# Performance work log

Measured on AMD Instinct MI355X. Metric: run time of the kernel, lower is better.

The kernel has to match this reference:

```python
import jax, jax.numpy as jnp
import numpy as np

B, N, C, Q, H, RATIO = 8, 8700, 256, 300, 8, 4
D = C // H
HID = C * RATIO
EPS = 1e-5


def _ln(x, w, b):
    m = jnp.mean(x, axis=-1, keepdims=True)
    v = jnp.mean((x - m) ** 2, axis=-1, keepdims=True)
    return (x - m) * jax.lax.rsqrt(v + EPS) * w + b


def setup_inputs() -> dict:
    key = jax.random.key(0)
    ks = jax.random.split(key, 8)
    s = 0.02
    return {
        "x": jax.random.normal(ks[0], (B, N, C), jnp.float32),
        # linear weights stored [in, out] (y = x @ W), no biases (qkv_bias=False, Mlp bias=False)
        "Wq": jax.random.normal(ks[1], (C, C), jnp.float32) * s,
        "Wk": jax.random.normal(ks[2], (C, C), jnp.float32) * s,
        "Wv": jax.random.normal(ks[3], (C, C), jnp.float32) * s,
        "Wp": jax.random.normal(ks[4], (C, C), jnp.float32) * s,
        "W1": jax.random.normal(ks[5], (C, HID), jnp.float32) * s,
        "W2": jax.random.normal(ks[6], (HID, C), jnp.float32) * s,
        "ln1_w": jnp.ones((C,), jnp.float32),
        "ln1_b": jnp.zeros((C,), jnp.float32),
        "ln2_w": jnp.ones((C,), jnp.float32),
        "ln2_b": jnp.zeros((C,), jnp.float32),
        "gamma1": jnp.ones((C,), jnp.float32),
        "gamma2": jnp.ones((C,), jnp.float32),
    }


def reference(x, Wq, Wk, Wv, Wp, W1, W2, ln1_w, ln1_b, ln2_w, ln2_b, gamma1, gamma2):
    scale = D ** -0.5
    xn = _ln(x, ln1_w, ln1_b)                       # [B,N,C]
    # SAQAttn: queries only from the first Q tokens; keys/values from all N tokens
    q = (xn[:, :Q] @ Wq).reshape(B, Q, H, D) * scale  # [B,Q,H,D]
    k = (xn @ Wk).reshape(B, N, H, D)
    v = (xn @ Wv).reshape(B, N, H, D)
    attn = jax.nn.softmax(jnp.einsum('bqhd,bnhd->bhqn', q, k), axis=-1)  # [B,H,Q,N]
    x_det = jnp.einsum('bhqn,bnhd->bqhd', attn, v).reshape(B, Q, C) @ Wp  # [B,Q,C]
    # residual with layer-scale gamma1; context tokens pass normed features through
    x_attn = jnp.concatenate([x_det, xn[:, Q:]], axis=1)
    x = x + gamma1 * x_attn
    # tokens_norm=False: norm2 only on query tokens
    x = jnp.concatenate([_ln(x[:, :Q], ln2_w, ln2_b), x[:, Q:]], axis=1)
    # MLP on query tokens with layer-scale gamma2 (exact GELU, as nn.GELU default)
    det = gamma2 * (jax.nn.gelu(x[:, :Q] @ W1, approximate=False) @ W2)
    # faithful to source: x_res + cat([det, x[:,Q:]]) doubles the context tokens
    return x + jnp.concatenate([det, x[:, Q:]], axis=1)
```

## Files before the change

kernel.cpp:

```cpp
#include <hip/hip_runtime.h>

#define BB 8
#define NN 8700
#define CC 256
#define QQ 300
#define HH 8
#define DD 32
#define HIDN 1024
#define NSPLIT 16
#define TSTR (NSPLIT * 64)
#define KSLACK 1536
#define PADN (NN + KSLACK)

typedef unsigned short u16;
typedef __attribute__((ext_vector_type(8))) short short8;
typedef __attribute__((ext_vector_type(4))) float f32x4;

#define MFMA16(a, b, c) __builtin_amdgcn_mfma_f32_16x16x32_bf16((a), (b), (c), 0, 0, 0)

__device__ __forceinline__ unsigned int cvtpk(float lo, float hi) {
    unsigned int r;
    asm("v_cvt_pk_bf16_f32 %0, %1, %2" : "=v"(r) : "v"(lo), "v"(hi));
    return r;
}
__device__ __forceinline__ u16 f2b_hw(float f) { return (u16)cvtpk(f, 0.f); }
__device__ __forceinline__ float b2f(u16 u) {
    unsigned int x = ((unsigned int)u) << 16;
    return __builtin_bit_cast(float, x);
}
__device__ __forceinline__ void gload16(const u16* g, u16* l) {
    __builtin_amdgcn_global_load_lds(
        (const __attribute__((address_space(1))) void*)g,
        (__attribute__((address_space(3))) void*)l, 16, 0, 0);
}

__global__ __launch_bounds__(256)
void prep_k(const float* __restrict__ x, const float* __restrict__ ln1w,
            const float* __restrict__ ln1b, const float* __restrict__ g1,
            u16* __restrict__ xn, float* __restrict__ out,
            const float* __restrict__ Wq, const float* __restrict__ Wk,
            const float* __restrict__ Wv, const float* __restrict__ Wp,
            const float* __restrict__ W1, const float* __restrict__ W2,
            u16* __restrict__ wdst, float qscale)
{
    __shared__ u16 tl[64][66];
    if (blockIdx.x < 17400) {
        int row = blockIdx.x * 4 + (threadIdx.x >> 6);
        int l = threadIdx.x & 63;
        size_t base = (size_t)row * CC + l * 4;
        float4 xv = *reinterpret_cast<const float4*>(x + base);
        float s  = xv.x + xv.y + xv.z + xv.w;
        float s2 = xv.x * xv.x + xv.y * xv.y + xv.z * xv.z + xv.w * xv.w;
#pragma unroll
        for (int m = 1; m < 64; m <<= 1) {
            s  += __shfl_xor(s,  m, 64);
            s2 += __shfl_xor(s2, m, 64);
        }
        float mean = s * (1.0f / CC);
        float rs = rsqrtf(s2 * (1.0f / CC) - mean * mean + 1e-5f);
        float4 wv = *reinterpret_cast<const float4*>(ln1w + l * 4);
        float4 bb = *reinterpret_cast<const float4*>(ln1b + l * 4);
        float n0 = (xv.x - mean) * rs * wv.x + bb.x;
        float n1 = (xv.y - mean) * rs * wv.y + bb.y;
        float n2 = (xv.z - mean) * rs * wv.z + bb.z;
        float n3 = (xv.w - mean) * rs * wv.w + bb.w;
        uint2 u; u.x = cvtpk(n0, n1); u.y = cvtpk(n2, n3);
        *reinterpret_cast<uint2*>(xn + base) = u;
        int n = row % NN;
        if (n >= QQ) {
            float4 gv = *reinterpret_cast<const float4*>(g1 + l * 4);
            float4 o;
            o.x = 2.0f * (xv.x + gv.x * n0);
            o.y = 2.0f * (xv.y + gv.y * n1);
            o.z = 2.0f * (xv.z + gv.z * n2);
            o.w = 2.0f * (xv.w + gv.w * n3);
            *reinterpret_cast<float4*>(out + base) = o;
        }
    } else {
        int bid = blockIdx.x - 17400;
        const float* src; int K, N, tr, tc; size_t dof; float sc = 1.f;
        if (bid < 64) {
            int mat = bid >> 4, ti = bid & 15;
            src = (mat == 0) ? Wq : (mat == 1) ? Wk : (mat == 2) ? Wv : Wp;
            K = 256; N = 256; tr = ti >> 2; tc = ti & 3;
            dof = (size_t)mat * 65536;
            if (mat == 0) sc = qscale;
        } else if (bid < 128) {
            int ti = bid - 64; src = W1; K = 256; N = 1024; tr = ti >> 4; tc = ti & 15; dof = 262144;
        } else {
            int ti = bid - 128; src = W2; K = 1024; N = 256; tr = ti >> 2; tc = ti & 3; dof = 524288;
        }
        int tid = threadIdx.x;
        int jj = tid & 63;
        int i0 = tid >> 6;
#pragma unroll
        for (int ii = 0; ii < 16; ii++) {
            int kk = i0 * 16 + ii;
            float v = src[(size_t)(tr * 64 + kk) * N + tc * 64 + jj] * sc;
            tl[kk][jj] = f2b_hw(v);
        }
        __syncthreads();
#pragma unroll
        for (int ii = 0; ii < 16; ii++) {
            int nn = i0 * 16 + ii;
            wdst[dof + (size_t)(tc * 64 + nn) * K + tr * 64 + jj] = tl[jj][nn];
        }
    }
}

__global__ __launch_bounds__(512)
void gemm_kv(const u16* __restrict__ A, const u16* __restrict__ WT,
             u16* __restrict__ Cb, u16* __restrict__ Cb2, int M)
{
    __shared__ u16 alds[64 * 256];
    const int tid = threadIdx.x;
    const int w = tid >> 6, l = tid & 63;
    const int l15 = l & 15, kg = l >> 4;
    const int rowbase = blockIdx.x * 64;
    const f32x4 fz = {0.f, 0.f, 0.f, 0.f};

    {
        const char* gb = (const char*)(A + (size_t)rowbase * CC);
        char* lb = (char*)alds;
#pragma unroll
        for (int j = 0; j < 4; j++) {
            int o = tid * 64 + j * 16;
            short8 v = *reinterpret_cast<const short8*>(gb + o);
            int d = o ^ (((o >> 9) & 7) << 4);
            *reinterpret_cast<short8*>(lb + d) = v;
        }
    }
    __syncthreads();

    const int colbase = w * 64;
    const u16* bp[4];
#pragma unroll
    for (int ni = 0; ni < 4; ni++)
        bp[ni] = WT + (size_t)(colbase + ni * 16 + l15) * CC + kg * 8;

    f32x4 acc[4][4];
#pragma unroll
    for (int mi = 0; mi < 4; mi++)
#pragma unroll
        for (int ni = 0; ni < 4; ni++) acc[mi][ni] = fz;

    const char* lb = (const char*)alds;
    const int sw = (l15 & 7) << 4;
    int abase[4];
#pragma unroll
    for (int mi = 0; mi < 4; mi++) abase[mi] = (mi * 16 + l15) << 9;

#pragma unroll
    for (int ks = 0; ks < 8; ks++) {
        const int koff = ((ks * 64) + (kg * 16)) ^ sw;
        short8 a[4], bfr[4];
#pragma unroll
        for (int mi = 0; mi < 4; mi++)
            a[mi] = *reinterpret_cast<const short8*>(lb + abase[mi] + koff);
#pragma unroll
        for (int ni = 0; ni < 4; ni++)
            bfr[ni] = *reinterpret_cast<const short8*>(bp[ni] + ks * 32);
#pragma unroll
        for (int mi = 0; mi < 4; mi++)
#pragma unroll
            for (int ni = 0; ni < 4; ni++)
                acc[mi][ni] = MFMA16(bfr[ni], a[mi], acc[mi][ni]);
    }

#pragma unroll
    for (int mi = 0; mi < 4; mi++) {
        int r = rowbase + mi * 16 + l15;
        if (r >= M) continue;
        int bb = r / NN, n = r - bb * NN;
#pragma unroll
        for (int ni = 0; ni < 4; ni++) {
            int col0 = colbase + ni * 16 + kg * 4;
            f32x4 v = acc[mi][ni];
            uint2 pk; pk.x = cvtpk(v[0], v[1]); pk.y = cvtpk(v[2], v[3]);
            int c = (col0 < CC) ? col0 : col0 - CC;
            int hb = (c >> 5) * BB + bb;
            size_t off = ((size_t)hb * PADN + n) * DD + (c & 31);
            if (col0 < CC) *reinterpret_cast<uint2*>(Cb  + off) = pk;
            else           *reinterpret_cast<uint2*>(Cb2 + off) = pk;
        }
    }
}

__global__ __launch_bounds__(256)
void gemm_q(const u16* __restrict__ A, const u16* __restrict__ WT, u16* __restrict__ Cb, int M)
{
    const int w = threadIdx.x >> 6, l = threadIdx.x & 63;
    const int l15 = l & 15, kg = l >> 4;
    const int rowbase = blockIdx.x * 16;
    const int colbase = w * 64;
    const short8 z8 = {0, 0, 0, 0, 0, 0, 0, 0};
    const f32x4 fz = {0.f, 0.f, 0.f, 0.f};

    int r = rowbase + l15;
    bool av = (r < M);
    int rr = av ? r : 0;
    const u16* ap = A + ((size_t)(rr / QQ) * NN + (rr % QQ)) * CC + kg * 8;
    const u16* bp[4];
#pragma unroll
    for (int ni = 0; ni < 4; ni++)
        bp[ni] = WT + (size_t)(colbase + ni * 16 + l15) * CC + kg * 8;

    f32x4 acc[4];
#pragma unroll
    for (int ni = 0; ni < 4; ni++) acc[ni] = fz;

    for (int ks = 0; ks < CC; ks += 32) {
        short8 a = av ? *reinterpret_cast<const short8*>(ap + ks) : z8;
#pragma unroll
        for (int ni = 0; ni < 4; ni++) {
            short8 bfr = *reinterpret_cast<const short8*>(bp[ni] + ks);
            acc[ni] = MFMA16(bfr, a, acc[ni]);
        }
    }
    if (r < M) {
        int bb = r / QQ, q = r - bb * QQ;
#pragma unroll
        for (int ni = 0; ni < 4; ni++) {
            int col0 = colbase + ni * 16 + kg * 4;
            uint2 pk; pk.x = cvtpk(acc[ni][0], acc[ni][1]); pk.y = cvtpk(acc[ni][2], acc[ni][3]);
            int hb = (col0 >> 5) * BB + bb;
            *reinterpret_cast<uint2*>(Cb + ((size_t)hb * QQ + q) * DD + (col0 & 31)) = pk;
        }
    }
}

__global__ __launch_bounds__(256)
void attn_k(const u16* __restrict__ qm, const u16* __restrict__ km,
            const u16* __restrict__ vm, u16* __restrict__ Opb,
            float* __restrict__ lp)
{
    __shared__ u16 klds[2][64 * 32];
    __shared__ u16 vt[2][32 * 64];
    __shared__ u16 plds[4][2][16 * 64];

    const int bx = blockIdx.x;
    const int split = bx >> 6;
    const int rem = bx & 63;
    const int h = rem >> 3, b = rem & 7;
    const int bh = b * HH + h;
    const int hb = h * BB + b;
    const int tid = threadIdx.x;
    const int w = tid >> 6, l = tid & 63;
    const int l15 = l & 15, kg = l >> 4;
    const int tstart = split * 64;
    const int nt = (NN - tstart + TSTR - 1) / TSTR;

    const f32x4 fz = {0.f, 0.f, 0.f, 0.f};
    const short os = (short)0x3F80;
    const short8 ones = {os, os, os, os, os, os, os, os};

    const u16* kbase = km + (size_t)hb * PADN * DD;
    const u16* vbase = vm + (size_t)hb * PADN * DD;
    const u16* qbase = qm + (size_t)hb * QQ * DD;
    const int vkp = (tid & 31) * 2;
    const int vdg = (tid >> 5) * 4;

    const int krow  = (w << 4) + (l >> 2);
    const int kslot = (l & 3) ^ ((krow >> 1) & 3);
    const u16* ksrc = kbase + krow * DD + kslot * 8;

    short8 qfr[5];
#pragma unroll
    for (int qf = 0; qf < 5; qf++) {
        int qrow = w * 80 + qf * 16 + l15;
        int qc = qrow < QQ ? qrow : 0;
        qfr[qf] = *reinterpret_cast<const short8*>(qbase + (size_t)qc * DD + kg * 8);
    }

    f32x4 o[2][5]; float lpart[5];
#pragma unroll
    for (int qf = 0; qf < 5; qf++) { o[0][qf] = fz; o[1][qf] = fz; lpart[qf] = 0.f; }

    gload16(ksrc + (size_t)tstart * DD, (u16*)((char*)klds[0] + (w << 10)));
    ushort4 v0r = *reinterpret_cast<const ushort4*>(vbase + (size_t)(tstart + vkp) * DD + vdg);
    ushort4 v1r = *reinterpret_cast<const ushort4*>(vbase + (size_t)(tstart + vkp + 1) * DD + vdg);

    char* pl = (char*)plds[w];
    const int rdswz = ((l15 << 7) ^ ((l15 & 7) << 4)) + (kg << 4);
    const int wrbase = (l15 << 7) ^ ((l15 & 7) << 4);

    for (int t = 0; t < nt; ++t) {
        const int n0 = tstart + t * TSTR;
        char* vtb = (char*)vt[t & 1];
#pragma unroll
        for (int i = 0; i < 4; i++) {
            int row = vdg + i;
            unsigned int pk2 = (unsigned int)v0r[i] | ((unsigned int)v1r[i] << 16);
            int byteo = ((row << 7) + (vkp << 1)) ^ ((row & 7) << 4);
            *reinterpret_cast<unsigned int*>(vtb + byteo) = pk2;
        }
        __syncthreads();

        gload16(ksrc + (size_t)(n0 + TSTR) * DD, (u16*)((char*)klds[(t + 1) & 1] + (w << 10)));
        ushort4 v0n = *reinterpret_cast<const ushort4*>(vbase + (size_t)(n0 + TSTR + vkp) * DD + vdg);
        ushort4 v1n = *reinterpret_cast<const ushort4*>(vbase + (size_t)(n0 + TSTR + vkp + 1) * DD + vdg);

        short8 kf[4];
        { const char* klb = (const char*)klds[t & 1];
#pragma unroll
          for (int kb = 0; kb < 4; kb++) {
              int row = kb * 16 + l15;
              int off = (row << 6) + ((kg ^ ((row >> 1) & 3)) << 4);
              kf[kb] = *reinterpret_cast<const short8*>(klb + off);
          } }

        short8 va[2][2];
#pragma unroll
        for (int ks = 0; ks < 2; ks++)
#pragma unroll
            for (int dg = 0; dg < 2; dg++) {
                int row = dg * 16 + l15;
                int byteo = ((row << 7) + 64 * ks + 16 * kg) ^ ((row & 7) << 4);
                va[ks][dg] = *reinterpret_cast<const short8*>(vtb + byteo);
            }

        const bool tail = (n0 + 64 > NN);

#pragma unroll
        for (int qf = 0; qf < 5; qf++) {
            short8 bp0, bp1;
            if (qf > 0) {
                const char* plr = pl + (((qf - 1) & 1) << 11);
                bp0 = *reinterpret_cast<const short8*>(plr + rdswz);
                bp1 = *reinterpret_cast<const short8*>(plr + rdswz + 64);
            }
            f32x4 s[4];
            __builtin_amdgcn_s_setprio(1);
#pragma unroll
            for (int kb = 0; kb < 4; kb++)
                s[kb] = MFMA16(kf[kb], qfr[qf], fz);
            __builtin_amdgcn_s_setprio(0);
            char* plw = pl + ((qf & 1) << 11);
#pragma unroll
            for (int kb = 0; kb < 4; kb++) {
                float p0 = exp2f(s[kb][0]);
                float p1 = exp2f(s[kb][1]);
                float p2 = exp2f(s[kb][2]);
                float p3 = exp2f(s[kb][3]);
                if (tail) {
                    int kbase2 = n0 + 16 * kb + 4 * kg;
                    if (kbase2 + 0 >= NN) p0 = 0.f;
                    if (kbase2 + 1 >= NN) p1 = 0.f;
                    if (kbase2 + 2 >= NN) p2 = 0.f;
                    if (kbase2 + 3 >= NN) p3 = 0.f;
                }
                uint2 pw; pw.x = cvtpk(p0, p1); pw.y = cvtpk(p2, p3);
                *reinterpret_cast<uint2*>(plw + (wrbase + ((16 * kb + 4 * kg) << 1))) = pw;
            }
            if (qf > 0) {
                __builtin_amdgcn_s_setprio(1);
                o[0][qf - 1] = MFMA16(va[0][0], bp0, o[0][qf - 1]);
                o[1][qf - 1] = MFMA16(va[0][1], bp0, o[1][qf - 1]);
                o[0][qf - 1] = MFMA16(va[1][0], bp1, o[0][qf - 1]);
                o[1][qf - 1] = MFMA16(va[1][1], bp1, o[1][qf - 1]);
                f32x4 tsum = MFMA16(ones, bp0, fz);
                tsum = MFMA16(ones, bp1, tsum);
                __builtin_amdgcn_s_setprio(0);
                lpart[qf - 1] += tsum[0];
            }
        }
        {
            const char* plr = pl + 0;
            short8 bp0 = *reinterpret_cast<const short8*>(plr + rdswz);
            short8 bp1 = *reinterpret_cast<const short8*>(plr + rdswz + 64);
            __builtin_amdgcn_s_setprio(1);
            o[0][4] = MFMA16(va[0][0], bp0, o[0][4]);
            o[1][4] = MFMA16(va[0][1], bp0, o[1][4]);
            o[0][4] = MFMA16(va[1][0], bp1, o[0][4]);
            o[1][4] = MFMA16(va[1][1], bp1, o[1][4]);
            f32x4 tsum = MFMA16(ones, bp0, fz);
            tsum = MFMA16(ones, bp1, tsum);
            __builtin_amdgcn_s_setprio(0);
            lpart[4] += tsum[0];
        }
        v0r = v0n; v1r = v1n;
    }

    size_t pb = (size_t)(split * 64 + bh) * QQ;
#pragma unroll
    for (int qf = 0; qf < 5; qf++) {
        int q = w * 80 + qf * 16 + l15;
        if (q >= QQ) continue;
        size_t pr = pb + q;
        if (kg == 0) lp[pr] = lpart[qf];
        uint2 w0; w0.x = cvtpk(o[0][qf][0], o[0][qf][1]); w0.y = cvtpk(o[0][qf][2], o[0][qf][3]);
        uint2 w1; w1.x = cvtpk(o[1][qf][0], o[1][qf][1]); w1.y = cvtpk(o[1][qf][2], o[1][qf][3]);
        *reinterpret_cast<uint2*>(Opb + pr * DD + kg * 4)      = w0;
        *reinterpret_cast<uint2*>(Opb + pr * DD + 16 + kg * 4) = w1;
    }
}

__global__ __launch_bounds__(256)
void cpl_k(const u16* __restrict__ Opb, const float* __restrict__ lp,
           const u16* __restrict__ WpT, const float* __restrict__ x,
           const float* __restrict__ g1, const float* __restrict__ w2,
           const float* __restrict__ b2, float* __restrict__ xqf, u16* __restrict__ xqb)
{
    __shared__ u16 albs[16 * 256];
    __shared__ float pdl[16][260];

    const int tid = threadIdx.x;
    const int r0 = blockIdx.x * 16;

    {
        int row = tid >> 4, cg = tid & 15;
        int r = r0 + row;
        int b = r / QQ, q = r - b * QQ;
        int h = cg >> 1;
        int dbase = (cg & 1) * 16;
        float acc[16];
#pragma unroll
        for (int j = 0; j < 16; j++) acc[j] = 0.f;
        float L = 0.f;
        for (int s = 0; s < NSPLIT; s++) {
            size_t pr = ((size_t)(s * 64) + b * 8 + h) * QQ + q;
            L += lp[pr];
            short8 v0 = *reinterpret_cast<const short8*>(Opb + pr * DD + dbase);
            short8 v1 = *reinterpret_cast<const short8*>(Opb + pr * DD + dbase + 8);
#pragma unroll
            for (int j = 0; j < 8; j++) {
                acc[j]     += b2f((u16)v0[j]);
                acc[8 + j] += b2f((u16)v1[j]);
            }
        }
        float inv = 1.0f / L;
        short8 o0, o1;
#pragma unroll
        for (int j = 0; j < 4; j++) {
            unsigned int a = cvtpk(acc[2 * j] * inv, acc[2 * j + 1] * inv);
            unsigned int bq = cvtpk(acc[8 + 2 * j] * inv, acc[9 + 2 * j] * inv);
            o0[2 * j] = (short)(a & 0xffff); o0[2 * j + 1] = (short)(a >> 16);
            o1[2 * j] = (short)(bq & 0xffff); o1[2 * j + 1] = (short)(bq >> 16);
        }
        char* lb = (char*)albs;
        int byte0 = (row << 9) + (cg << 5);
        *reinterpret_cast<short8*>(lb + ((byte0)      ^ ((row & 7) << 4))) = o0;
        *reinterpret_cast<short8*>(lb + ((byte0 + 16) ^ ((row & 7) << 4))) = o1;
    }
    __syncthreads();

    const int w = tid >> 6, l = tid & 63;
    const int l15 = l & 15, kg = l >> 4;
    {
        const f32x4 fz = {0.f, 0.f, 0.f, 0.f};
        const int colbase = w * 64;
        const u16* bp[4];
#pragma unroll
        for (int ni = 0; ni < 4; ni++)
            bp[ni] = WpT + (size_t)(colbase + ni * 16 + l15) * CC + kg * 8;
        f32x4 acc[4];
#pragma unroll
        for (int ni = 0; ni < 4; ni++) acc[ni] = fz;
        const char* lb = (const char*)albs;
        const int arow = l15 << 9;
        const int sw = (l15 & 7) << 4;
#pragma unroll
        for (int ks = 0; ks < 8; ks++) {
            short8 a = *reinterpret_cast<const short8*>(lb + (arow + ((kg * 16 + ks * 64) ^ sw)));
#pragma unroll
            for (int ni = 0; ni < 4; ni++) {
                short8 bfr = *reinterpret_cast<const short8*>(bp[ni] + ks * 32);
                acc[ni] = MFMA16(bfr, a, acc[ni]);
            }
        }
#pragma unroll
        for (int ni = 0; ni < 4; ni++) {
            float4 v; v.x = acc[ni][0]; v.y = acc[ni][1]; v.z = acc[ni][2]; v.w = acc[ni][3];
            *reinterpret_cast<float4*>(&pdl[l15][colbase + ni * 16 + kg * 4]) = v;
        }
    }
    __syncthreads();

    {
        int row = tid >> 4, cg = tid & 15;
        int r = r0 + row;
        int b = r / QQ, q = r - b * QQ;
        size_t xoff = ((size_t)b * NN + q) * CC + cg * 16;
        float val[16];
        float s = 0.f, s2 = 0.f;
#pragma unroll
        for (int j4 = 0; j4 < 4; j4++) {
            float4 xv = *reinterpret_cast<const float4*>(x + xoff + j4 * 4);
            float4 gv = *reinterpret_cast<const float4*>(g1 + cg * 16 + j4 * 4);
            int c = cg * 16 + j4 * 4;
            val[j4 * 4 + 0] = xv.x + gv.x * pdl[row][c + 0];
            val[j4 * 4 + 1] = xv.y + gv.y * pdl[row][c + 1];
            val[j4 * 4 + 2] = xv.z + gv.z * pdl[row][c + 2];
            val[j4 * 4 + 3] = xv.w + gv.w * pdl[row][c + 3];
#pragma unroll
            for (int j = 0; j < 4; j++) {
                float v = val[j4 * 4 + j];
                s += v; s2 += v * v;
            }
        }
#pragma unroll
        for (int m = 1; m < 16; m <<= 1) {
            s  += __shfl_xor(s,  m, 64);
            s2 += __shfl_xor(s2, m, 64);
        }
        float mean = s * (1.0f / CC);
        float rs = rsqrtf(s2 * (1.0f / CC) - mean * mean + 1e-5f);
        size_t roff = (size_t)r * CC + cg * 16;
#pragma unroll
        for (int j4 = 0; j4 < 4; j4++) {
            int c = cg * 16 + j4 * 4;
            float4 wv = *reinterpret_cast<const float4*>(w2 + c);
            float4 bb = *reinterpret_cast<const float4*>(b2 + c);
            float n0 = (val[j4 * 4 + 0] - mean) * rs * wv.x + bb.x;
            float n1 = (val[j4 * 4 + 1] - mean) * rs * wv.y + bb.y;
            float n2 = (val[j4 * 4 + 2] - mean) * rs * wv.z + bb.z;
            float n3 = (val[j4 * 4 + 3] - mean) * rs * wv.w + bb.w;
            float4 o; o.x = n0; o.y = n1; o.z = n2; o.w = n3;
            *reinterpret_cast<float4*>(xqf + roff + j4 * 4) = o;
            uint2 u; u.x = cvtpk(n0, n1); u.y = cvtpk(n2, n3);
            *reinterpret_cast<uint2*>(xqb + roff + j4 * 4) = u;
        }
    }
}

__global__ __launch_bounds__(256)
void mlp_k(const u16* __restrict__ xqb, const u16* __restrict__ W1T,
           const u16* __restrict__ W2T, const float* __restrict__ xqf,
           const float* __restrict__ g2, float* __restrict__ out)
{
    __shared__ u16 h1l[16 * 1024];

    const int tid = threadIdx.x;
    const int w = tid >> 6, l = tid & 63;
    const int l15 = l & 15, kg = l >> 4;
    const int r0 = blockIdx.x * 16;
    const f32x4 fz = {0.f, 0.f, 0.f, 0.f};

    {
        const u16* ap = xqb + (size_t)(r0 + l15) * CC + kg * 8;
        f32x4 acc[16];
#pragma unroll
        for (int ni = 0; ni < 16; ni++) acc[ni] = fz;
#pragma unroll
        for (int ks = 0; ks < 8; ks++) {
            short8 a = *reinterpret_cast<const short8*>(ap + ks * 32);
#pragma unroll
            for (int ni = 0; ni < 16; ni++) {
                const u16* bp = W1T + (size_t)(w * 256 + ni * 16 + l15) * CC + kg * 8 + ks * 32;
                short8 bfr = *reinterpret_cast<const short8*>(bp);
                acc[ni] = MFMA16(bfr, a, acc[ni]);
            }
        }
        char* lb = (char*)h1l;
        const int sw = (l15 & 7) << 4;
#pragma unroll
        for (int ni = 0; ni < 16; ni++) {
            float g0 = 0.5f * acc[ni][0] * (1.0f + erff(acc[ni][0] * 0.70710678118654752f));
            float g1v = 0.5f * acc[ni][1] * (1.0f + erff(acc[ni][1] * 0.70710678118654752f));
            float g2v = 0.5f * acc[ni][2] * (1.0f + erff(acc[ni][2] * 0.70710678118654752f));
            float g3 = 0.5f * acc[ni][3] * (1.0f + erff(acc[ni][3] * 0.70710678118654752f));
            uint2 pk; pk.x = cvtpk(g0, g1v); pk.y = cvtpk(g2v, g3);
            int byteo = (l15 << 11) + (((w * 256 + ni * 16 + kg * 4) << 1) ^ sw);
            *reinterpret_cast<uint2*>(lb + byteo) = pk;
        }
    }
    __syncthreads();

    {
        const int colbase = w * 64;
        const u16* bp[4];
#pragma unroll
        for (int ni = 0; ni < 4; ni++)
            bp[ni] = W2T + (size_t)(colbase + ni * 16 + l15) * HIDN + kg * 8;
        f32x4 acc[4];
#pragma unroll
        for (int ni = 0; ni < 4; ni++) acc[ni] = fz;
        const char* lb = (const char*)h1l;
        const int arow = l15 << 11;
        const int sw = (l15 & 7) << 4;
#pragma unroll
        for (int ks = 0; ks < 32; ks++) {
            short8 a = *reinterpret_cast<const short8*>(lb + arow + (((kg * 8 + ks * 32) << 1) ^ sw));
#pragma unroll
            for (int ni = 0; ni < 4; ni++) {
                short8 bfr = *reinterpret_cast<const short8*>(bp[ni] + ks * 32);
                acc[ni] = MFMA16(bfr, a, acc[ni]);
            }
        }
        int r = r0 + l15;
        size_t orow = (size_t)(r / QQ) * NN + (r % QQ);
#pragma unroll
        for (int ni = 0; ni < 4; ni++) {
            int col0 = colbase + ni * 16 + kg * 4;
            float4 xv = *reinterpret_cast<const float4*>(xqf + (size_t)r * CC + col0);
            float4 gv = *reinterpret_cast<const float4*>(g2 + col0);
            float4 o;
            o.x = xv.x + gv.x * acc[ni][0];
            o.y = xv.y + gv.y * acc[ni][1];
            o.z = xv.z + gv.z * acc[ni][2];
            o.w = xv.w + gv.w * acc[ni][3];
            *reinterpret_cast<float4*>(out + orow * CC + col0) = o;
        }
    }
}

extern "C" void kernel_launch(void* const* d_in, const int* in_sizes, int n_in,
                              void* d_out, int out_size, void* d_ws, size_t ws_size,
                              hipStream_t stream)
{
    (void)in_sizes; (void)n_in; (void)out_size; (void)ws_size;
    const float* x    = (const float*)d_in[0];
    const float* Wq   = (const float*)d_in[1];
    const float* Wk   = (const float*)d_in[2];
    const float* Wv   = (const float*)d_in[3];
    const float* Wp   = (const float*)d_in[4];
    const float* W1   = (const float*)d_in[5];
    const float* W2   = (const float*)d_in[6];
    const float* ln1w = (const float*)d_in[7];
    const float* ln1b = (const float*)d_in[8];
    const float* ln2w = (const float*)d_in[9];
    const float* ln2b = (const float*)d_in[10];
    const float* g1   = (const float*)d_in[11];
    const float* g2   = (const float*)d_in[12];
    float* out = (float*)d_out;

    char* p = (char*)d_ws;
    auto alloc = [&](size_t bytes) { char* r = p; p += (bytes + 255) & ~(size_t)255; return r; };

    const size_t MKV = (size_t)BB * NN;
    const size_t MQ  = (size_t)BB * QQ;

    u16* WqT  = (u16*)alloc((size_t)CC * CC * 2);
    u16* WkvT = (u16*)alloc((size_t)CC * CC * 2 * 2);
    u16* WpT  = (u16*)alloc((size_t)CC * CC * 2);
    u16* W1T  = (u16*)alloc((size_t)CC * HIDN * 2);
    u16* W2T  = (u16*)alloc((size_t)HIDN * CC * 2);
    u16* xn   = (u16*)alloc((MKV + 64) * CC * 2);
    u16* kbf  = (u16*)alloc((size_t)64 * PADN * DD * 2);
    u16* vbf  = (u16*)alloc((size_t)64 * PADN * DD * 2);
    u16* qbf  = (u16*)alloc((size_t)64 * QQ * DD * 2);
    u16* xqb  = (u16*)alloc(MQ * CC * 2);
    float* xqf = (float*)alloc(MQ * CC * 4);
    u16* Opb  = (u16*)alloc((size_t)NSPLIT * 64 * QQ * DD * 2);
    float* lp  = (float*)alloc((size_t)NSPLIT * 64 * QQ * 4);

    const float qscale = 0.17677669529663687f * 1.4426950408889634f;

    prep_k<<<17592, 256, 0, stream>>>(x, ln1w, ln1b, g1, xn, out,
                                      Wq, Wk, Wv, Wp, W1, W2, WqT, qscale);

    gemm_kv<<<1088, 512, 0, stream>>>(xn, WkvT, kbf, vbf, (int)MKV);
    gemm_q<<<150, 256, 0, stream>>>(xn, WqT, qbf, (int)MQ);

    attn_k<<<64 * NSPLIT, 256, 0, stream>>>(qbf, kbf, vbf, Opb, lp);

    cpl_k<<<150, 256, 0, stream>>>(Opb, lp, WpT, x, g1, ln2w, ln2b, xqf, xqb);

    mlp_k<<<150, 256, 0, stream>>>(xqb, W1T, W2T, xqf, g2, out);
}
```

Baseline: 219.4 us.

## Deepen software pipeline of QK, exp and PV stages across query fragments

Restructures the per-tile attention loop into a three-stage software pipeline. The QK MFMAs for fragment qf run alongside exp2/convert/LDS write for fragment qf-1 and the PV MFMAs for fragment qf-2, instead of a two-stage overlap. The aim is to hide the latency of exp and LDS round-trips behind matrix-core work. It costs extra live registers for the carried scores and adds drain code after the loop, which may hurt occupancy.

```diff
diff --git a/kernel.cpp b/kernel.cpp
--- a/kernel.cpp
+++ b/kernel.cpp
@@ -321,27 +321,65 @@
 
         const bool tail = (n0 + 64 > NN);
 
+        f32x4 sp[4];
 #pragma unroll
         for (int qf = 0; qf < 5; qf++) {
-            short8 bp0, bp1;
-            if (qf > 0) {
-                const char* plr = pl + (((qf - 1) & 1) << 11);
-                bp0 = *reinterpret_cast<const short8*>(plr + rdswz);
-                bp1 = *reinterpret_cast<const short8*>(plr + rdswz + 64);
-            }
-            f32x4 s[4];
+            short8 pb0, pb1;
+            if (qf >= 2) {
+                const char* plr = pl + (((qf - 2) & 1) << 11);
+                pb0 = *reinterpret_cast<const short8*>(plr + rdswz);
+                pb1 = *reinterpret_cast<const short8*>(plr + rdswz + 64);
+            }
+            f32x4 sc[4];
             __builtin_amdgcn_s_setprio(1);
 #pragma unroll
             for (int kb = 0; kb < 4; kb++)
-                s[kb] = MFMA16(kf[kb], qfr[qf], fz);
+                sc[kb] = MFMA16(kf[kb], qfr[qf], fz);
             __builtin_amdgcn_s_setprio(0);
-            char* plw = pl + ((qf & 1) << 11);
+            if (qf >= 1) {
+                char* plw = pl + (((qf - 1) & 1) << 11);
+#pragma unroll
+                for (int kb = 0; kb < 4; kb++) {
+                    float p0 = exp2f(sp[kb][0]);
+                    float p1 = exp2f(sp[kb][1]);
+                    float p2 = exp2f(sp[kb][2]);
+                    float p3 = exp2f(sp[kb][3]);
+                    if (tail) {
+                        int kbase2 = n0 + 16 * kb + 4 * kg;
+                        if (kbase2 + 0 >= NN) p0 = 0.f;
+                        if (kbase2 + 1 >= NN) p1 = 0.f;
+                        if (kbase2 + 2 >= NN) p2 = 0.f;
+                        if (kbase2 + 3 >= NN) p3 = 0.f;
+                    }
+                    uint2 pw; pw.x = cvtpk(p0, p1); pw.y = cvtpk(p2, p3);
+                    *reinterpret_cast<uint2*>(plw + (wrbase + ((16 * kb + 4 * kg) << 1))) = pw;
+                }
+            }
+            if (qf >= 2) {
+                __builtin_amdgcn_s_setprio(1);
+                o[0][qf - 2] = MFMA16(va[0][0], pb0, o[0][qf - 2]);
+                o[1][qf - 2] = MFMA16(va[0][1], pb0, o[1][qf - 2]);
+                o[0][qf - 2] = MFMA16(va[1][0], pb1, o[0][qf - 2]);
+                o[1][qf - 2] = MFMA16(va[1][1], pb1, o[1][qf - 2]);
+                f32x4 tsum = MFMA16(ones, pb0, fz);
+                tsum = MFMA16(ones, pb1, tsum);
+                __builtin_amdgcn_s_setprio(0);
+                lpart[qf - 2] += tsum[0];
+            }
+#pragma unroll
+            for (int kb = 0; kb < 4; kb++) sp[kb] = sc[kb];
+        }
+        {
+            const char* plr = pl + (1 << 11);
+            short8 pb0 = *reinterpret_cast<const short8*>(plr + rdswz);
+            short8 pb1 = *reinterpret_cast<const short8*>(plr + rdswz + 64);
+            char* plw = pl + 0;
 #pragma unroll
             for (int kb = 0; kb < 4; kb++) {
-                float p0 = exp2f(s[kb][0]);
-                float p1 = exp2f(s[kb][1]);
-                float p2 = exp2f(s[kb][2]);
-                float p3 = exp2f(s[kb][3]);
+                float p0 = exp2f(sp[kb][0]);
+                float p1 = exp2f(sp[kb][1]);
+                float p2 = exp2f(sp[kb][2]);
+                float p3 = exp2f(sp[kb][3]);
                 if (tail) {
                     int kbase2 = n0 + 16 * kb + 4 * kg;
                     if (kbase2 + 0 >= NN) p0 = 0.f;
@@ -352,29 +390,27 @@
                 uint2 pw; pw.x = cvtpk(p0, p1); pw.y = cvtpk(p2, p3);
                 *reinterpret_cast<uint2*>(plw + (wrbase + ((16 * kb + 4 * kg) << 1))) = pw;
             }
-            if (qf > 0) {
-                __builtin_amdgcn_s_setprio(1);
-                o[0][qf - 1] = MFMA16(va[0][0], bp0, o[0][qf - 1]);
-                o[1][qf - 1] = MFMA16(va[0][1], bp0, o[1][qf - 1]);
-                o[0][qf - 1] = MFMA16(va[1][0], bp1, o[0][qf - 1]);
-                o[1][qf - 1] = MFMA16(va[1][1], bp1, o[1][qf - 1]);
-                f32x4 tsum = MFMA16(ones, bp0, fz);
-                tsum = MFMA16(ones, bp1, tsum);
-                __builtin_amdgcn_s_setprio(0);
-                lpart[qf - 1] += tsum[0];
-            }
+            __builtin_amdgcn_s_setprio(1);
+            o[0][3] = MFMA16(va[0][0], pb0, o[0][3]);
+            o[1][3] = MFMA16(va[0][1], pb0, o[1][3]);
+            o[0][3] = MFMA16(va[1][0], pb1, o[0][3]);
+            o[1][3] = MFMA16(va[1][1], pb1, o[1][3]);
+            f32x4 tsum = MFMA16(ones, pb0, fz);
+            tsum = MFMA16(ones, pb1, tsum);
+            __builtin_amdgcn_s_setprio(0);
+            lpart[3] += tsum[0];
         }
         {
             const char* plr = pl + 0;
-            short8 bp0 = *reinterpret_cast<const short8*>(plr + rdswz);
-            short8 bp1 = *reinterpret_cast<const short8*>(plr + rdswz + 64);
+            short8 pb0 = *reinterpret_cast<const short8*>(plr + rdswz);
+            short8 pb1 = *reinterpret_cast<const short8*>(plr + rdswz + 64);
             __builtin_amdgcn_s_setprio(1);
-            o[0][4] = MFMA16(va[0][0], bp0, o[0][4]);
-            o[1][4] = MFMA16(va[0][1], bp0, o[1][4]);
-            o[0][4] = MFMA16(va[1][0], bp1, o[0][4]);
-            o[1][4] = MFMA16(va[1][1], bp1, o[1][4]);
-            f32x4 tsum = MFMA16(ones, bp0, fz);
-            tsum = MFMA16(ones, bp1, tsum);
+            o[0][4] = MFMA16(va[0][0], pb0, o[0][4]);
+            o[1][4] = MFMA16(va[0][1], pb0, o[1][4]);
+            o[0][4] = MFMA16(va[1][0], pb1, o[0][4]);
+            o[1][4] = MFMA16(va[1][1], pb1, o[1][4]);
+            f32x4 tsum = MFMA16(ones, pb0, fz);
+            tsum = MFMA16(ones, pb1, tsum);
             __builtin_amdgcn_s_setprio(0);
             lpart[4] += tsum[0];
         }
```

Result: no change. 218.5 us, median of 2 (-0.4%).
